# Performance work log

Hardware: AMD Instinct MI355X
Metric: run time of the kernel (lower is better)

## Reference

```python
import jax, jax.numpy as jnp
import numpy as np

EMBED = 256
HEAD = 64
B, T = 16, 2048


def setup_inputs() -> dict:
    key = jax.random.key(0)
    kq, kk, kv, kwq, kwk, kwv = jax.random.split(key, 6)
    q = jax.random.normal(kq, (B, T, EMBED), dtype=jnp.float32)
    k = jax.random.normal(kk, (B, T, EMBED), dtype=jnp.float32)
    v = jax.random.normal(kv, (B, T, EMBED), dtype=jnp.float32)
    # causal mask matching the module's tril buffer semantics, broadcast over batch
    mask = jnp.tril(jnp.ones((T, T), dtype=jnp.int32))[None, :, :]
    s = 1.0 / np.sqrt(EMBED)
    Wq = (jax.random.normal(kwq, (EMBED, HEAD), dtype=jnp.float32) * s)
    Wk = (jax.random.normal(kwk, (EMBED, HEAD), dtype=jnp.float32) * s)
    Wv = (jax.random.normal(kwv, (EMBED, HEAD), dtype=jnp.float32) * s)
    return {"q": q, "k": k, "v": v, "mask": mask, "Wq": Wq, "Wk": Wk, "Wv": Wv}


def reference(q, k, v, mask, Wq, Wk, Wv):
    # projections (bias-free Linear): [B,T,E] @ [E,H] -> [B,T,H]
    C = k.shape[-1]
    qh = jnp.einsum('bte,eh->bth', q, Wq)
    kh = jnp.einsum('bte,eh->bth', k, Wk)
    vh = jnp.einsum('bte,eh->bth', v, Wv)
    # scores scaled by C**-0.5 (input embed dim, as in the source)
    wei = jnp.einsum('bth,bsh->bts', qh, kh) * (C ** -0.5)
    wei = jnp.where(mask == 0, -jnp.inf, wei)
    wei = jax.nn.softmax(wei, axis=-1)
    # dropout is identity in eval mode
    out = jnp.einsum('bts,bsh->bth', wei, vh)
    return out
```

## Files before the change

kernel.cpp:

```cpp
#include <hip/hip_runtime.h>
#include <hip/hip_bf16.h>
#include <cstdint>


#define NB 16
#define TT 2048
#define EE 256
#define HH 64

using bf16x8 = __attribute__((ext_vector_type(8))) __bf16;
using f32x4  = __attribute__((ext_vector_type(4))) float;
using u16x4  = __attribute__((ext_vector_type(4))) unsigned short;

static __device__ __forceinline__ unsigned short f2b(float f) {
  return __builtin_bit_cast(unsigned short, (__bf16)f);
}

__global__ __launch_bounds__(256) void prep_w_kernel(
    const float* __restrict__ Wq, const float* __restrict__ Wk,
    const float* __restrict__ Wv, unsigned short* __restrict__ wt) {
  int o = blockIdx.x * 256 + threadIdx.x;
  int p = o >> 14, rem = o & 16383;
  int n = rem >> 8, kk = rem & 255;
  const float* W = (p == 0) ? Wq : ((p == 1) ? Wk : Wv);
  float val = W[kk * HH + n];
  if (p == 0) val *= 0.0625f;
  wt[o] = f2b(val);
}

__global__ __launch_bounds__(256) void proj_kernel(
    const float* __restrict__ qi, const float* __restrict__ ki, const float* __restrict__ vi,
    const unsigned short* __restrict__ wt,
    unsigned short* __restrict__ qh, unsigned short* __restrict__ kh,
    unsigned short* __restrict__ vt) {
  const int p = blockIdx.y;
  const int row0 = blockIdx.x * 64;
  const float* __restrict__ src = (p == 0) ? qi : ((p == 1) ? ki : vi);
  const unsigned short* __restrict__ wp = wt + p * (HH * EE);

  __shared__ unsigned short A[64 * EE];
  const int tid = threadIdx.x;

  #pragma unroll
  for (int i = 0; i < 16; ++i) {
    int c = i * 256 + tid;
    int r = c >> 6, d4 = c & 63;
    float4 f = *reinterpret_cast<const float4*>(src + (size_t)(row0 + r) * EE + d4 * 4);
    u16x4 h = { f2b(f.x), f2b(f.y), f2b(f.z), f2b(f.w) };
    int byte = r * 512 + ((d4 * 8) ^ ((r & 7) << 4));
    *reinterpret_cast<u16x4*>(reinterpret_cast<char*>(A) + byte) = h;
  }
  __syncthreads();

  const int wv = tid >> 6, lane = tid & 63, lr = lane & 15, lg = lane >> 4;
  f32x4 acc[4] = {};
  const int arow = wv * 16 + lr;
  const char* Abase = reinterpret_cast<const char*>(A) + arow * 512;
  #pragma unroll
  for (int k0 = 0; k0 < EE; k0 += 32) {
    bf16x8 af = *reinterpret_cast<const bf16x8*>(
        Abase + ((k0 * 2 + lg * 16) ^ ((arow & 7) << 4)));
    #pragma unroll
    for (int nt = 0; nt < 4; ++nt) {
      bf16x8 bfm = *reinterpret_cast<const bf16x8*>(wp + (nt * 16 + lr) * EE + k0 + lg * 8);
      acc[nt] = __builtin_amdgcn_mfma_f32_16x16x32_bf16(af, bfm, acc[nt], 0, 0, 0);
    }
  }

  if (p < 2) {
    unsigned short* dst = (p == 0) ? qh : kh;
    #pragma unroll
    for (int nt = 0; nt < 4; ++nt)
      #pragma unroll
      for (int r = 0; r < 4; ++r) {
        int grow = row0 + wv * 16 + lg * 4 + r;
        dst[(size_t)grow * HH + nt * 16 + lr] = f2b(acc[nt][r]);
      }
  } else {
    __syncthreads();
    #pragma unroll
    for (int nt = 0; nt < 4; ++nt)
      #pragma unroll
      for (int r = 0; r < 4; ++r) {
        int col = nt * 16 + lr;
        int trow = wv * 16 + lg * 4 + r;
        *reinterpret_cast<unsigned short*>(reinterpret_cast<char*>(A)
            + col * 128 + ((trow * 2) ^ ((col & 7) << 4))) = f2b(acc[nt][r]);
      }
    __syncthreads();
    const int bb = row0 >> 11, t0 = row0 & 2047;
    #pragma unroll
    for (int i = 0; i < 2; ++i) {
      int ch = i * 256 + tid;
      int col = ch >> 3, ro = (ch & 7) * 8;
      bf16x8 val = *reinterpret_cast<const bf16x8*>(reinterpret_cast<char*>(A)
          + col * 128 + ((ro * 2) ^ ((col & 7) << 4)));
      *reinterpret_cast<bf16x8*>(vt + (size_t)(bb * 64 + col) * TT + t0 + ro) = val;
    }
  }
}

__global__ __launch_bounds__(256) void attn_kernel(
    const unsigned short* __restrict__ qh, const unsigned short* __restrict__ kh,
    const unsigned short* __restrict__ vt, float* __restrict__ out) {
  __shared__ unsigned short K_lds[64 * 64];
  __shared__ unsigned short V_lds[64 * 64];
  __shared__ unsigned short P_lds[4 * 16 * 64];

  const int bid = blockIdx.x;
  const int u = bid >> 1, odd = bid & 1;
  const int b = u >> 4, j = u & 15;
  const int qt = odd ? j : 31 - j;
  const int q0 = qt * 64;
  const int tid = threadIdx.x, wv = tid >> 6, lane = tid & 63, lr = lane & 15, lg = lane >> 4;

  bf16x8 qf[2];
  {
    const unsigned short* qrow = qh + ((size_t)b * TT + q0 + wv * 16 + lr) * HH;
    qf[0] = *reinterpret_cast<const bf16x8*>(qrow + lg * 8);
    qf[1] = *reinterpret_cast<const bf16x8*>(qrow + 32 + lg * 8);
  }

  f32x4 oa[4] = {};
  float m[4] = {-__builtin_inff(), -__builtin_inff(), -__builtin_inff(), -__builtin_inff()};
  float ld[4] = {0.f, 0.f, 0.f, 0.f};

  for (int kt = 0; kt <= qt; ++kt) {
    __syncthreads();
    #pragma unroll
    for (int i = 0; i < 2; ++i) {
      int ch = i * 256 + tid;
      int rr = ch >> 3, off8 = (ch & 7) * 8;
      bf16x8 kvv = *reinterpret_cast<const bf16x8*>(
          kh + ((size_t)b * TT + kt * 64 + rr) * HH + off8);
      *reinterpret_cast<bf16x8*>(reinterpret_cast<char*>(K_lds)
          + rr * 128 + ((off8 * 2) ^ ((rr & 7) << 4))) = kvv;
      bf16x8 vvv = *reinterpret_cast<const bf16x8*>(
          vt + (size_t)(b * 64 + rr) * TT + kt * 64 + off8);
      *reinterpret_cast<bf16x8*>(reinterpret_cast<char*>(V_lds)
          + rr * 128 + ((off8 * 2) ^ ((rr & 7) << 4))) = vvv;
    }
    __syncthreads();

    f32x4 s[4] = {};
    #pragma unroll
    for (int ks = 0; ks < 2; ++ks)
      #pragma unroll
      for (int nt = 0; nt < 4; ++nt) {
        int key = nt * 16 + lr;
        bf16x8 kf = *reinterpret_cast<const bf16x8*>(reinterpret_cast<const char*>(K_lds)
            + key * 128 + ((ks * 64 + lg * 16) ^ ((key & 7) << 4)));
        s[nt] = __builtin_amdgcn_mfma_f32_16x16x32_bf16(qf[ks], kf, s[nt], 0, 0, 0);
      }

    if (kt == qt) {
      #pragma unroll
      for (int nt = 0; nt < 4; ++nt)
        #pragma unroll
        for (int r = 0; r < 4; ++r)
          if (nt * 16 + lr > wv * 16 + lg * 4 + r) s[nt][r] = -__builtin_inff();
    }

    float corr[4];
    #pragma unroll
    for (int r = 0; r < 4; ++r) {
      float t = fmaxf(fmaxf(s[0][r], s[1][r]), fmaxf(s[2][r], s[3][r]));
      t = fmaxf(t, __shfl_xor(t, 1));
      t = fmaxf(t, __shfl_xor(t, 2));
      t = fmaxf(t, __shfl_xor(t, 4));
      t = fmaxf(t, __shfl_xor(t, 8));
      float mn = fmaxf(m[r], t);
      corr[r] = __expf(m[r] - mn);
      m[r] = mn;
    }
    #pragma unroll
    for (int nt = 0; nt < 4; ++nt)
      #pragma unroll
      for (int r = 0; r < 4; ++r)
        s[nt][r] = __expf(s[nt][r] - m[r]);
    #pragma unroll
    for (int r = 0; r < 4; ++r) {
      float t = s[0][r] + s[1][r] + s[2][r] + s[3][r];
      t += __shfl_xor(t, 1);
      t += __shfl_xor(t, 2);
      t += __shfl_xor(t, 4);
      t += __shfl_xor(t, 8);
      ld[r] = ld[r] * corr[r] + t;
      oa[0][r] *= corr[r]; oa[1][r] *= corr[r]; oa[2][r] *= corr[r]; oa[3][r] *= corr[r];
    }

    char* pbase = reinterpret_cast<char*>(P_lds) + wv * 2048;
    #pragma unroll
    for (int nt = 0; nt < 4; ++nt)
      #pragma unroll
      for (int r = 0; r < 4; ++r) {
        int row = lg * 4 + r;
        *reinterpret_cast<unsigned short*>(pbase
            + row * 128 + (((nt * 16 + lr) * 2) ^ ((row & 7) << 4))) = f2b(s[nt][r]);
      }

    #pragma unroll
    for (int ks = 0; ks < 2; ++ks) {
      bf16x8 pf = *reinterpret_cast<const bf16x8*>(
          pbase + lr * 128 + ((ks * 64 + lg * 16) ^ ((lr & 7) << 4)));
      #pragma unroll
      for (int nt = 0; nt < 4; ++nt) {
        int dim = nt * 16 + lr;
        bf16x8 vf = *reinterpret_cast<const bf16x8*>(reinterpret_cast<const char*>(V_lds)
            + dim * 128 + ((ks * 64 + lg * 16) ^ ((dim & 7) << 4)));
        oa[nt] = __builtin_amdgcn_mfma_f32_16x16x32_bf16(pf, vf, oa[nt], 0, 0, 0);
      }
    }
  }

  #pragma unroll
  for (int r = 0; r < 4; ++r) {
    float inv = 1.0f / ld[r];
    #pragma unroll
    for (int nt = 0; nt < 4; ++nt) {
      int row = q0 + wv * 16 + lg * 4 + r;
      out[((size_t)b * TT + row) * HH + nt * 16 + lr] = oa[nt][r] * inv;
    }
  }
}

extern "C" void kernel_launch(void* const* d_in, const int* in_sizes, int n_in,
                              void* d_out, int out_size, void* d_ws, size_t ws_size,
                              hipStream_t stream) {
  const float* q  = (const float*)d_in[0];
  const float* k  = (const float*)d_in[1];
  const float* v  = (const float*)d_in[2];
  const float* Wq = (const float*)d_in[4];
  const float* Wk = (const float*)d_in[5];
  const float* Wv = (const float*)d_in[6];

  char* ws = (char*)d_ws;
  unsigned short* wt = (unsigned short*)ws;
  unsigned short* qh = (unsigned short*)(ws + 98304);
  unsigned short* kh = qh + (size_t)NB * TT * HH;
  unsigned short* vt = kh + (size_t)NB * TT * HH;
  float* out = (float*)d_out;

  prep_w_kernel<<<192, 256, 0, stream>>>(Wq, Wk, Wv, wt);
  proj_kernel<<<dim3(512, 3), 256, 0, stream>>>(q, k, v, wt, qh, kh, vt);
  attn_kernel<<<512, 256, 0, stream>>>(qh, kh, vt, out);
}
```

Before: 220.9 us.

## Split key tiles across wave pairs and read K/V directly from global

Each block now covers two 16-row query blocks, paired light and heavy for causal balance. Two waves share each query block and take alternating key tiles, then merge their partial softmax states (max, sum, output) through LDS at the end. K and V are read straight from global memory into MFMA fragments instead of being staged in LDS, which removes the per-tile barriers. The cost is more global and L2 traffic, since the waves no longer share K/V through LDS, plus a final merge step; the grid doubles to 1024 blocks.

```diff
diff --git a/kernel.cpp b/kernel.cpp
--- a/kernel.cpp
+++ b/kernel.cpp
@@ -103,62 +103,51 @@
 __global__ __launch_bounds__(256) void attn_kernel(
     const unsigned short* __restrict__ qh, const unsigned short* __restrict__ kh,
     const unsigned short* __restrict__ vt, float* __restrict__ out) {
-  __shared__ unsigned short K_lds[64 * 64];
-  __shared__ unsigned short V_lds[64 * 64];
-  __shared__ unsigned short P_lds[4 * 16 * 64];
+  __shared__ float O_lds[2][16][64];
+  __shared__ float M_lds[2][16], L_lds[2][16];
+  __shared__ unsigned short P_lds[4][1024];
+
+  const int tid = threadIdx.x;
+  const int wv = tid >> 6, lane = tid & 63, lr = lane & 15, lg = lane >> 4;
+  const int pr = wv >> 1, sub = wv & 1;
 
   const int bid = blockIdx.x;
-  const int u = bid >> 1, odd = bid & 1;
-  const int b = u >> 4, j = u & 15;
-  const int qt = odd ? j : 31 - j;
-  const int q0 = qt * 64;
-  const int tid = threadIdx.x, wv = tid >> 6, lane = tid & 63, lr = lane & 15, lg = lane >> 4;
-
-  bf16x8 qf[2];
-  {
-    const unsigned short* qrow = qh + ((size_t)b * TT + q0 + wv * 16 + lr) * HH;
-    qf[0] = *reinterpret_cast<const bf16x8*>(qrow + lg * 8);
-    qf[1] = *reinterpret_cast<const bf16x8*>(qrow + 32 + lg * 8);
-  }
+  const int b = bid >> 6, i = bid & 63;
+  const int qb = pr ? (127 - i) : i;
+  const int row0 = qb * 16;
+  const int ntile = (qb >> 2) + 1;
+  const int ktd = ntile - 1;
+
+  const unsigned short* qrow = qh + ((size_t)b * TT + row0 + lr) * HH;
+  bf16x8 qf0 = *reinterpret_cast<const bf16x8*>(qrow + lg * 8);
+  bf16x8 qf1 = *reinterpret_cast<const bf16x8*>(qrow + 32 + lg * 8);
+
+  const unsigned short* kb = kh + (size_t)b * TT * HH;
+  const unsigned short* vb = vt + (size_t)b * HH * TT;
+  char* pbase = reinterpret_cast<char*>(P_lds[wv]);
 
   f32x4 oa[4] = {};
   float m[4] = {-__builtin_inff(), -__builtin_inff(), -__builtin_inff(), -__builtin_inff()};
   float ld[4] = {0.f, 0.f, 0.f, 0.f};
 
-  for (int kt = 0; kt <= qt; ++kt) {
-    __syncthreads();
-    #pragma unroll
-    for (int i = 0; i < 2; ++i) {
-      int ch = i * 256 + tid;
-      int rr = ch >> 3, off8 = (ch & 7) * 8;
-      bf16x8 kvv = *reinterpret_cast<const bf16x8*>(
-          kh + ((size_t)b * TT + kt * 64 + rr) * HH + off8);
-      *reinterpret_cast<bf16x8*>(reinterpret_cast<char*>(K_lds)
-          + rr * 128 + ((off8 * 2) ^ ((rr & 7) << 4))) = kvv;
-      bf16x8 vvv = *reinterpret_cast<const bf16x8*>(
-          vt + (size_t)(b * 64 + rr) * TT + kt * 64 + off8);
-      *reinterpret_cast<bf16x8*>(reinterpret_cast<char*>(V_lds)
-          + rr * 128 + ((off8 * 2) ^ ((rr & 7) << 4))) = vvv;
-    }
-    __syncthreads();
+  for (int kt = sub; kt < ntile; kt += 2) {
+    const unsigned short* kp = kb + (size_t)kt * 64 * HH;
 
     f32x4 s[4] = {};
     #pragma unroll
-    for (int ks = 0; ks < 2; ++ks)
-      #pragma unroll
-      for (int nt = 0; nt < 4; ++nt) {
-        int key = nt * 16 + lr;
-        bf16x8 kf = *reinterpret_cast<const bf16x8*>(reinterpret_cast<const char*>(K_lds)
-            + key * 128 + ((ks * 64 + lg * 16) ^ ((key & 7) << 4)));
-        s[nt] = __builtin_amdgcn_mfma_f32_16x16x32_bf16(qf[ks], kf, s[nt], 0, 0, 0);
-      }
-
-    if (kt == qt) {
+    for (int nt = 0; nt < 4; ++nt) {
+      bf16x8 kf0 = *reinterpret_cast<const bf16x8*>(kp + (nt * 16 + lr) * HH + lg * 8);
+      bf16x8 kf1 = *reinterpret_cast<const bf16x8*>(kp + (nt * 16 + lr) * HH + 32 + lg * 8);
+      s[nt] = __builtin_amdgcn_mfma_f32_16x16x32_bf16(qf0, kf0, s[nt], 0, 0, 0);
+      s[nt] = __builtin_amdgcn_mfma_f32_16x16x32_bf16(qf1, kf1, s[nt], 0, 0, 0);
+    }
+
+    if (kt == ktd) {
       #pragma unroll
       for (int nt = 0; nt < 4; ++nt)
         #pragma unroll
         for (int r = 0; r < 4; ++r)
-          if (nt * 16 + lr > wv * 16 + lg * 4 + r) s[nt][r] = -__builtin_inff();
+          if (kt * 64 + nt * 16 + lr > row0 + lg * 4 + r) s[nt][r] = -__builtin_inff();
     }
 
     float corr[4];
@@ -189,7 +178,6 @@
       oa[0][r] *= corr[r]; oa[1][r] *= corr[r]; oa[2][r] *= corr[r]; oa[3][r] *= corr[r];
     }
 
-    char* pbase = reinterpret_cast<char*>(P_lds) + wv * 2048;
     #pragma unroll
     for (int nt = 0; nt < 4; ++nt)
       #pragma unroll
@@ -205,21 +193,41 @@
           pbase + lr * 128 + ((ks * 64 + lg * 16) ^ ((lr & 7) << 4)));
       #pragma unroll
       for (int nt = 0; nt < 4; ++nt) {
-        int dim = nt * 16 + lr;
-        bf16x8 vf = *reinterpret_cast<const bf16x8*>(reinterpret_cast<const char*>(V_lds)
-            + dim * 128 + ((ks * 64 + lg * 16) ^ ((dim & 7) << 4)));
+        bf16x8 vf = *reinterpret_cast<const bf16x8*>(
+            vb + (size_t)(nt * 16 + lr) * TT + kt * 64 + ks * 32 + lg * 8);
         oa[nt] = __builtin_amdgcn_mfma_f32_16x16x32_bf16(pf, vf, oa[nt], 0, 0, 0);
       }
     }
   }
 
-  #pragma unroll
-  for (int r = 0; r < 4; ++r) {
-    float inv = 1.0f / ld[r];
-    #pragma unroll
-    for (int nt = 0; nt < 4; ++nt) {
-      int row = q0 + wv * 16 + lg * 4 + r;
-      out[((size_t)b * TT + row) * HH + nt * 16 + lr] = oa[nt][r] * inv;
+  if (sub == 1) {
+    #pragma unroll
+    for (int nt = 0; nt < 4; ++nt)
+      #pragma unroll
+      for (int r = 0; r < 4; ++r)
+        O_lds[pr][lg * 4 + r][nt * 16 + lr] = oa[nt][r];
+    if (lr == 0) {
+      #pragma unroll
+      for (int r = 0; r < 4; ++r) {
+        M_lds[pr][lg * 4 + r] = m[r];
+        L_lds[pr][lg * 4 + r] = ld[r];
+      }
+    }
+  }
+  __syncthreads();
+  if (sub == 0) {
+    #pragma unroll
+    for (int r = 0; r < 4; ++r) {
+      int row = lg * 4 + r;
+      float m1 = M_lds[pr][row], l1 = L_lds[pr][row];
+      float mm = fmaxf(m[r], m1);
+      float c0 = __expf(m[r] - mm), c1 = __expf(m1 - mm);
+      float inv = 1.0f / (ld[r] * c0 + l1 * c1);
+      #pragma unroll
+      for (int nt = 0; nt < 4; ++nt) {
+        float o = (oa[nt][r] * c0 + O_lds[pr][row][nt * 16 + lr] * c1) * inv;
+        out[((size_t)b * TT + row0 + row) * HH + nt * 16 + lr] = o;
+      }
     }
   }
 }
@@ -243,5 +251,5 @@
 
   prep_w_kernel<<<192, 256, 0, stream>>>(Wq, Wk, Wv, wt);
   proj_kernel<<<dim3(512, 3), 256, 0, stream>>>(q, k, v, wt, qh, kh, vt);
-  attn_kernel<<<512, 256, 0, stream>>>(qh, kh, vt, out);
-}
+  attn_kernel<<<1024, 256, 0, stream>>>(qh, kh, vt, out);
+}
```

Result: slower. 263.2 us (+19.2%).

## Double-buffer K/V tiles in attention with register prefetch and MFMA priority

Applied to the files above, without the earlier changes.

The attention kernel now keeps two LDS buffers for K and V. The next tile is loaded into registers at the start of each iteration and written to the other buffer after the PV matmul, which removes one barrier per iteration and hides global load latency behind compute. It also raises wave priority around the MFMA sections and reorders block-to-tile assignment so the first half of blocks takes the short causal rows and the second half the long ones. The projection kernel issues all 16 float4 loads before converting them, at the cost of extra registers.

```diff
diff --git a/kernel.cpp b/kernel.cpp
--- a/kernel.cpp
+++ b/kernel.cpp
@@ -41,12 +41,15 @@
   __shared__ unsigned short A[64 * EE];
   const int tid = threadIdx.x;
 
+  const float4* srcp = reinterpret_cast<const float4*>(src) + (size_t)row0 * (EE / 4);
+  float4 f[16];
+  #pragma unroll
+  for (int i = 0; i < 16; ++i) f[i] = srcp[i * 256 + tid];
   #pragma unroll
   for (int i = 0; i < 16; ++i) {
     int c = i * 256 + tid;
     int r = c >> 6, d4 = c & 63;
-    float4 f = *reinterpret_cast<const float4*>(src + (size_t)(row0 + r) * EE + d4 * 4);
-    u16x4 h = { f2b(f.x), f2b(f.y), f2b(f.z), f2b(f.w) };
+    u16x4 h = { f2b(f[i].x), f2b(f[i].y), f2b(f[i].z), f2b(f[i].w) };
     int byte = r * 512 + ((d4 * 8) ^ ((r & 7) << 4));
     *reinterpret_cast<u16x4*>(reinterpret_cast<char*>(A) + byte) = h;
   }
@@ -103,55 +106,76 @@
 __global__ __launch_bounds__(256) void attn_kernel(
     const unsigned short* __restrict__ qh, const unsigned short* __restrict__ kh,
     const unsigned short* __restrict__ vt, float* __restrict__ out) {
-  __shared__ unsigned short K_lds[64 * 64];
-  __shared__ unsigned short V_lds[64 * 64];
-  __shared__ unsigned short P_lds[4 * 16 * 64];
+  __shared__ unsigned short K_lds[2][64 * 64];
+  __shared__ unsigned short V_lds[2][64 * 64];
+  __shared__ unsigned short P_lds[4][1024];
+
+  const int tid = threadIdx.x;
+  const int wv = tid >> 6, lane = tid & 63, lr = lane & 15, lg = lane >> 4;
 
   const int bid = blockIdx.x;
-  const int u = bid >> 1, odd = bid & 1;
-  const int b = u >> 4, j = u & 15;
-  const int qt = odd ? j : 31 - j;
+  const int half = bid >> 8, j = bid & 255;
+  const int b = j >> 4;
+  const int qt = half ? (31 - (j & 15)) : (j & 15);
   const int q0 = qt * 64;
-  const int tid = threadIdx.x, wv = tid >> 6, lane = tid & 63, lr = lane & 15, lg = lane >> 4;
-
-  bf16x8 qf[2];
-  {
-    const unsigned short* qrow = qh + ((size_t)b * TT + q0 + wv * 16 + lr) * HH;
-    qf[0] = *reinterpret_cast<const bf16x8*>(qrow + lg * 8);
-    qf[1] = *reinterpret_cast<const bf16x8*>(qrow + 32 + lg * 8);
-  }
+
+  const unsigned short* qrow = qh + ((size_t)b * TT + q0 + wv * 16 + lr) * HH;
+  bf16x8 qf0 = *reinterpret_cast<const bf16x8*>(qrow + lg * 8);
+  bf16x8 qf1 = *reinterpret_cast<const bf16x8*>(qrow + 32 + lg * 8);
+
+  const unsigned short* kb = kh + (size_t)b * TT * HH;
+  const unsigned short* vb = vt + (size_t)b * HH * TT;
+  char* pbase = reinterpret_cast<char*>(P_lds[wv]);
+
+  const int rr0 = tid >> 3, of0 = (tid & 7) * 8;
+  const int rr1 = (256 + tid) >> 3, of1 = (tid & 7) * 8;
+  bf16x8 kr0, kr1, vr0, vr1;
+
+#define LOADKV(kt_) do {                                                         \
+    const unsigned short* kp_ = kb + (size_t)(kt_) * 64 * HH;                    \
+    const unsigned short* vp_ = vb + (kt_) * 64;                                 \
+    kr0 = *reinterpret_cast<const bf16x8*>(kp_ + rr0 * HH + of0);                \
+    kr1 = *reinterpret_cast<const bf16x8*>(kp_ + rr1 * HH + of1);                \
+    vr0 = *reinterpret_cast<const bf16x8*>(vp_ + (size_t)rr0 * TT + of0);        \
+    vr1 = *reinterpret_cast<const bf16x8*>(vp_ + (size_t)rr1 * TT + of1);        \
+  } while (0)
+
+#define WRITEKV(bi_) do {                                                        \
+    *reinterpret_cast<bf16x8*>(reinterpret_cast<char*>(K_lds[bi_])              \
+        + rr0 * 128 + ((of0 * 2) ^ ((rr0 & 7) << 4))) = kr0;                     \
+    *reinterpret_cast<bf16x8*>(reinterpret_cast<char*>(K_lds[bi_])              \
+        + rr1 * 128 + ((of1 * 2) ^ ((rr1 & 7) << 4))) = kr1;                     \
+    *reinterpret_cast<bf16x8*>(reinterpret_cast<char*>(V_lds[bi_])              \
+        + rr0 * 128 + ((of0 * 2) ^ ((rr0 & 7) << 4))) = vr0;                     \
+    *reinterpret_cast<bf16x8*>(reinterpret_cast<char*>(V_lds[bi_])              \
+        + rr1 * 128 + ((of1 * 2) ^ ((rr1 & 7) << 4))) = vr1;                     \
+  } while (0)
 
   f32x4 oa[4] = {};
   float m[4] = {-__builtin_inff(), -__builtin_inff(), -__builtin_inff(), -__builtin_inff()};
-  float ld[4] = {0.f, 0.f, 0.f, 0.f};
+  float ldn[4] = {0.f, 0.f, 0.f, 0.f};
+
+  LOADKV(0);
+  WRITEKV(0);
+  __syncthreads();
 
   for (int kt = 0; kt <= qt; ++kt) {
-    __syncthreads();
-    #pragma unroll
-    for (int i = 0; i < 2; ++i) {
-      int ch = i * 256 + tid;
-      int rr = ch >> 3, off8 = (ch & 7) * 8;
-      bf16x8 kvv = *reinterpret_cast<const bf16x8*>(
-          kh + ((size_t)b * TT + kt * 64 + rr) * HH + off8);
-      *reinterpret_cast<bf16x8*>(reinterpret_cast<char*>(K_lds)
-          + rr * 128 + ((off8 * 2) ^ ((rr & 7) << 4))) = kvv;
-      bf16x8 vvv = *reinterpret_cast<const bf16x8*>(
-          vt + (size_t)(b * 64 + rr) * TT + kt * 64 + off8);
-      *reinterpret_cast<bf16x8*>(reinterpret_cast<char*>(V_lds)
-          + rr * 128 + ((off8 * 2) ^ ((rr & 7) << 4))) = vvv;
-    }
-    __syncthreads();
+    const int cb = kt & 1;
+    if (kt < qt) LOADKV(kt + 1);
 
     f32x4 s[4] = {};
+    __builtin_amdgcn_s_setprio(1);
     #pragma unroll
     for (int ks = 0; ks < 2; ++ks)
       #pragma unroll
       for (int nt = 0; nt < 4; ++nt) {
         int key = nt * 16 + lr;
-        bf16x8 kf = *reinterpret_cast<const bf16x8*>(reinterpret_cast<const char*>(K_lds)
+        bf16x8 kf = *reinterpret_cast<const bf16x8*>(
+            reinterpret_cast<const char*>(K_lds[cb])
             + key * 128 + ((ks * 64 + lg * 16) ^ ((key & 7) << 4)));
-        s[nt] = __builtin_amdgcn_mfma_f32_16x16x32_bf16(qf[ks], kf, s[nt], 0, 0, 0);
-      }
+        s[nt] = __builtin_amdgcn_mfma_f32_16x16x32_bf16(ks ? qf1 : qf0, kf, s[nt], 0, 0, 0);
+      }
+    __builtin_amdgcn_s_setprio(0);
 
     if (kt == qt) {
       #pragma unroll
@@ -185,11 +209,10 @@
       t += __shfl_xor(t, 2);
       t += __shfl_xor(t, 4);
       t += __shfl_xor(t, 8);
-      ld[r] = ld[r] * corr[r] + t;
+      ldn[r] = ldn[r] * corr[r] + t;
       oa[0][r] *= corr[r]; oa[1][r] *= corr[r]; oa[2][r] *= corr[r]; oa[3][r] *= corr[r];
     }
 
-    char* pbase = reinterpret_cast<char*>(P_lds) + wv * 2048;
     #pragma unroll
     for (int nt = 0; nt < 4; ++nt)
       #pragma unroll
@@ -199,6 +222,7 @@
             + row * 128 + (((nt * 16 + lr) * 2) ^ ((row & 7) << 4))) = f2b(s[nt][r]);
       }
 
+    __builtin_amdgcn_s_setprio(1);
     #pragma unroll
     for (int ks = 0; ks < 2; ++ks) {
       bf16x8 pf = *reinterpret_cast<const bf16x8*>(
@@ -206,22 +230,29 @@
       #pragma unroll
       for (int nt = 0; nt < 4; ++nt) {
         int dim = nt * 16 + lr;
-        bf16x8 vf = *reinterpret_cast<const bf16x8*>(reinterpret_cast<const char*>(V_lds)
+        bf16x8 vf = *reinterpret_cast<const bf16x8*>(
+            reinterpret_cast<const char*>(V_lds[cb])
             + dim * 128 + ((ks * 64 + lg * 16) ^ ((dim & 7) << 4)));
         oa[nt] = __builtin_amdgcn_mfma_f32_16x16x32_bf16(pf, vf, oa[nt], 0, 0, 0);
       }
     }
+    __builtin_amdgcn_s_setprio(0);
+
+    if (kt < qt) WRITEKV((kt + 1) & 1);
+    __syncthreads();
   }
 
   #pragma unroll
   for (int r = 0; r < 4; ++r) {
-    float inv = 1.0f / ld[r];
+    float inv = 1.0f / ldn[r];
     #pragma unroll
     for (int nt = 0; nt < 4; ++nt) {
       int row = q0 + wv * 16 + lg * 4 + r;
       out[((size_t)b * TT + row) * HH + nt * 16 + lr] = oa[nt][r] * inv;
     }
   }
+#undef LOADKV
+#undef WRITEKV
 }
 
 extern "C" void kernel_launch(void* const* d_in, const int* in_sizes, int n_in,
```

New measurement: 198.4 us. 10.2% less time.
